# Performance work log

Measured on AMD Instinct MI355X. Metric: run time of the kernel, lower is better.

Reference implementation:

```python
import jax, jax.numpy as jnp
import numpy as np


def setup_inputs() -> dict:
    key = jax.random.key(0)
    k1, k2, k3 = jax.random.split(key, 3)
    B, C, T = 16, 256, 1024
    inp = jax.random.normal(k1, (B, C, T), dtype=jnp.float32)
    tgt = jax.random.normal(k2, (B, C, T), dtype=jnp.float32)
    mask = jax.random.uniform(k3, (B, T), dtype=jnp.float32)
    return {"inp": inp, "tgt": tgt, "mask": mask}


def reference(inp, tgt, mask):
    # inp, tgt: (B, C, T); mask: (B, T)
    # permute(0,2,1) -> (B, T, C), then mask along T
    x = jnp.transpose(inp, (0, 2, 1)) * mask[:, :, None]  # (B, T, C)
    y = jnp.transpose(tgt, (0, 2, 1)) * mask[:, :, None]  # (B, T, C)
    xy = jnp.einsum('btc,bsc->bts', x, y)  # (B, T, T)
    xx = jnp.einsum('btc,bsc->bts', x, x)  # (B, T, T)
    yy = jnp.einsum('btc,bsc->bts', y, y)  # (B, T, T)
    similarity = 2.0 * xy / (xx + yy)
    loss = jnp.exp(-similarity)
    return jnp.mean(loss)
```

## Files before the change

kernel.cpp:

```cpp
#include <hip/hip_runtime.h>

constexpr int Bc = 16;
constexpr int Cc = 256;
constexpr int Tc = 1024;

typedef __attribute__((ext_vector_type(16))) float f32x16;

__global__ void zero_out_kernel(float* out) { out[0] = 0.0f; }

__device__ inline unsigned f2fp8(float x) {
    unsigned u = __float_as_uint(x);
    unsigned sign = (u >> 24) & 0x80u;
    unsigned au = u & 0x7fffffffu;
    if (au < 0x3c800000u) {
        float m = __uint_as_float(au) * 512.0f;
        unsigned d = (unsigned)(m + 0.5f);
        return (d > 7u) ? (sign | 0x08u) : (sign | d);
    }
    if (au > 0x43e00000u) au = 0x43e00000u;
    au += 0x7ffffu + ((au >> 20) & 1u);
    unsigned e = (au >> 23) - 120u;
    return sign | (e << 3) | ((au >> 20) & 7u);
}

__global__ __launch_bounds__(256) void convert_fp8_kernel(
    const float* __restrict__ inp, const float* __restrict__ tgt,
    unsigned char* __restrict__ PX, unsigned char* __restrict__ PY,
    float* __restrict__ out)
{
    if (blockIdx.x == 0 && threadIdx.x == 0) out[0] = 0.0f;

    __shared__ float tile[32][132];
    const int gid = blockIdx.x;
    const int a  = gid >> 10;
    const int b  = (gid >> 6) & 15;
    const int cs = (gid >> 3) & 7;
    const int tg = gid & 7;
    const int t0 = tg * 128;
    const int tid = threadIdx.x;

    const float* src = a ? tgt : inp;
    unsigned char* dst = a ? PY : PX;

#pragma unroll
    for (int i = 0; i < 4; ++i) {
        const int c  = i * 8 + (tid >> 5);
        const int t4 = (tid & 31) * 4;
        const float4 v = *(const float4*)&src[((size_t)(b * Cc + cs * 32 + c)) * Tc + t0 + t4];
        tile[c][t4 + 0] = v.x; tile[c][t4 + 1] = v.y;
        tile[c][t4 + 2] = v.z; tile[c][t4 + 3] = v.w;
    }
    __syncthreads();

    const int tb  = tid >> 6;
    const int kh  = (tid >> 5) & 1;
    const int row = tid & 31;
    const int t   = tb * 32 + row;
    unsigned un[4];
#pragma unroll
    for (int q = 0; q < 4; ++q) {
        unsigned wv = 0;
#pragma unroll
        for (int jj = 0; jj < 4; ++jj) {
            const int j  = q * 4 + jj;
            const int cp = kh * 8 + (j & 7) + (j >> 3) * 16;
            wv |= f2fp8(tile[cp][t]) << (jj * 8);
        }
        un[q] = wv;
    }
    const size_t off = ((size_t)((b * 8 + cs) * 32 + tg * 4 + tb)) * 1024
                     + kh * 512 + row * 16;
    *(uint4*)(dst + off) = make_uint4(un[0], un[1], un[2], un[3]);
}

#define GLDS16(g, l) __builtin_amdgcn_global_load_lds(               \
    (__attribute__((address_space(1))) void*)(g),                    \
    (__attribute__((address_space(3))) void*)(l), 16, 0, 0)

#define MF(a, b, c) c = __builtin_amdgcn_mfma_f32_32x32x16_fp8_fp8((a), (b), (c), 0, 0, 0)

__device__ inline float epi_sum(const f32x16& XY, const f32x16& SS) {
    float l = 0.0f;
#pragma unroll
    for (int i = 0; i < 16; ++i) {
        float s = 2.0f * XY[i] / SS[i];
        s = fminf(fmaxf(s, -60.0f), 60.0f);
        l += __expf(-s);
    }
    return l;
}

__global__ __launch_bounds__(256, 2) void jvs_fp8_kernel(
    const unsigned char* __restrict__ PX,
    const unsigned char* __restrict__ PY,
    float* __restrict__ out)
{
    __shared__ __align__(16) unsigned char lds[2][16384];

    const int gid = blockIdx.x;
    const int b   = gid >> 6;
    const int tb0 = ((gid >> 3) & 7) * 4;
    const int sb0 = (gid & 7) * 4;

    const int tid  = threadIdx.x;
    const int lane = tid & 63;
    const int w    = tid >> 6;
    const int wm   = (w >> 1) * 2;
    const int wn   = (w & 1) * 2;

    const unsigned char* gax = PX + ((size_t)(b * 8 * 32 + tb0)) * 1024 + tid * 16;
    const unsigned char* gay = PY + ((size_t)(b * 8 * 32 + tb0)) * 1024 + tid * 16;
    const unsigned char* gbx = PX + ((size_t)(b * 8 * 32 + sb0)) * 1024 + tid * 16;
    const unsigned char* gby = PY + ((size_t)(b * 8 * 32 + sb0)) * 1024 + tid * 16;

    const int fo = (lane >> 5) * 512 + (lane & 31) * 16;

    f32x16 z;
#pragma unroll
    for (int i = 0; i < 16; ++i) z[i] = 0.0f;
    f32x16 xy00 = z, xy01 = z, xy10 = z, xy11 = z;
    f32x16 ss00 = z, ss01 = z, ss10 = z, ss11 = z;

#define STAGE(bufi, cs)                                               \
    do {                                                              \
        unsigned char* L = lds[bufi];                                 \
        const size_t o = (size_t)(cs) * 32768;                        \
        GLDS16(gax + o, L +     0 + tid * 16);                        \
        GLDS16(gay + o, L +  4096 + tid * 16);                        \
        GLDS16(gbx + o, L +  8192 + tid * 16);                        \
        GLDS16(gby + o, L + 12288 + tid * 16);                        \
    } while (0)

    STAGE(0, 0);
    __syncthreads();

    for (int it = 0; it < 8; ++it) {
        if (it < 7) STAGE((it + 1) & 1, it + 1);
        const unsigned char* L = lds[it & 1];

        const long2 ax0 = *(const long2*)&L[(wm + 0) * 1024 + fo];
        const long2 ax1 = *(const long2*)&L[(wm + 1) * 1024 + fo];
        const long2 ay0 = *(const long2*)&L[4096 + (wm + 0) * 1024 + fo];
        const long2 ay1 = *(const long2*)&L[4096 + (wm + 1) * 1024 + fo];
        const long2 bx0 = *(const long2*)&L[8192 + (wn + 0) * 1024 + fo];
        const long2 bx1 = *(const long2*)&L[8192 + (wn + 1) * 1024 + fo];
        const long2 by0 = *(const long2*)&L[12288 + (wn + 0) * 1024 + fo];
        const long2 by1 = *(const long2*)&L[12288 + (wn + 1) * 1024 + fo];

        MF(ax0.x, bx0.x, ss00); MF(ax0.x, bx1.x, ss01);
        MF(ax1.x, bx0.x, ss10); MF(ax1.x, bx1.x, ss11);
        MF(ay0.x, by0.x, ss00); MF(ay0.x, by1.x, ss01);
        MF(ay1.x, by0.x, ss10); MF(ay1.x, by1.x, ss11);
        MF(ax0.x, by0.x, xy00); MF(ax0.x, by1.x, xy01);
        MF(ax1.x, by0.x, xy10); MF(ax1.x, by1.x, xy11);
        MF(ax0.y, bx0.y, ss00); MF(ax0.y, bx1.y, ss01);
        MF(ax1.y, bx0.y, ss10); MF(ax1.y, bx1.y, ss11);
        MF(ay0.y, by0.y, ss00); MF(ay0.y, by1.y, ss01);
        MF(ay1.y, by0.y, ss10); MF(ay1.y, by1.y, ss11);
        MF(ax0.y, by0.y, xy00); MF(ax0.y, by1.y, xy01);
        MF(ax1.y, by0.y, xy10); MF(ax1.y, by1.y, xy11);

        __syncthreads();
    }
#undef STAGE

    float local = epi_sum(xy00, ss00) + epi_sum(xy01, ss01)
                + epi_sum(xy10, ss10) + epi_sum(xy11, ss11);

#pragma unroll
    for (int off = 32; off > 0; off >>= 1)
        local += __shfl_down(local, off, 64);

    __shared__ float red[4];
    if (lane == 0) red[w] = local;
    __syncthreads();
    if (tid == 0)
        atomicAdd(out, (red[0] + red[1] + red[2] + red[3])
                       * (1.0f / ((float)Bc * (float)Tc * (float)Tc)));
}

constexpr int TILE = 64;
constexpr int KC   = 16;

__global__ __launch_bounds__(256) void jvs_loss_kernel(
    const float* __restrict__ inp, const float* __restrict__ tgt, float* __restrict__ out)
{
    __shared__ float xs_t[KC][TILE];
    __shared__ float xs_s[KC][TILE];
    __shared__ float ys_t[KC][TILE];
    __shared__ float ys_s[KC][TILE];

    constexpr int NT = Tc / TILE;
    const int blk = blockIdx.x;
    const int b   = blk / (NT * NT);
    const int r   = blk % (NT * NT);
    const int t0  = (r / NT) * TILE;
    const int s0  = (r % NT) * TILE;
    const int tid = threadIdx.x;
    const int tx  = tid & 15;
    const int ty  = tid >> 4;
    const int lrow  = tid >> 4;
    const int lcol4 = tid & 15;
    const float* baseI = inp + (size_t)b * Cc * Tc;
    const float* baseT = tgt + (size_t)b * Cc * Tc;

    float acc_xy[4][4] = {{0.f}}, acc_xx[4][4] = {{0.f}}, acc_yy[4][4] = {{0.f}};
    for (int c0 = 0; c0 < Cc; c0 += KC) {
        __syncthreads();
        const size_t rowOff = (size_t)(c0 + lrow) * Tc;
        *(float4*)&xs_t[lrow][lcol4 * 4] = *(const float4*)(baseI + rowOff + t0 + lcol4 * 4);
        *(float4*)&xs_s[lrow][lcol4 * 4] = *(const float4*)(baseI + rowOff + s0 + lcol4 * 4);
        *(float4*)&ys_t[lrow][lcol4 * 4] = *(const float4*)(baseT + rowOff + t0 + lcol4 * 4);
        *(float4*)&ys_s[lrow][lcol4 * 4] = *(const float4*)(baseT + rowOff + s0 + lcol4 * 4);
        __syncthreads();
#pragma unroll
        for (int kc = 0; kc < KC; ++kc) {
            float xt[4], xsv[4], yt[4], ysv[4];
#pragma unroll
            for (int i = 0; i < 4; ++i) {
                xt[i]  = xs_t[kc][ty * 4 + i];  yt[i]  = ys_t[kc][ty * 4 + i];
                xsv[i] = xs_s[kc][tx * 4 + i];  ysv[i] = ys_s[kc][tx * 4 + i];
            }
#pragma unroll
            for (int i = 0; i < 4; ++i)
#pragma unroll
                for (int j = 0; j < 4; ++j) {
                    acc_xy[i][j] += xt[i] * ysv[j];
                    acc_xx[i][j] += xt[i] * xsv[j];
                    acc_yy[i][j] += yt[i] * ysv[j];
                }
        }
    }
    float local = 0.0f;
#pragma unroll
    for (int i = 0; i < 4; ++i)
#pragma unroll
        for (int j = 0; j < 4; ++j) {
            float sim = 2.0f * acc_xy[i][j] / (acc_xx[i][j] + acc_yy[i][j]);
            sim = fminf(fmaxf(sim, -60.0f), 60.0f);
            local += __expf(-sim);
        }
#pragma unroll
    for (int off = 32; off > 0; off >>= 1) local += __shfl_down(local, off, 64);
    __shared__ float red[4];
    if ((tid & 63) == 0) red[tid >> 6] = local;
    __syncthreads();
    if (tid == 0)
        atomicAdd(out, (red[0] + red[1] + red[2] + red[3])
                       * (1.0f / ((float)Bc * (float)Tc * (float)Tc)));
}

extern "C" void kernel_launch(void* const* d_in, const int* in_sizes, int n_in,
                              void* d_out, int out_size, void* d_ws, size_t ws_size,
                              hipStream_t stream) {
    const float* inp = (const float*)d_in[0];
    const float* tgt = (const float*)d_in[1];
    float* out = (float*)d_out;

    const size_t oneP = (size_t)Bc * Cc * Tc;
    if (ws_size >= 2 * oneP) {
        unsigned char* PX = (unsigned char*)d_ws;
        unsigned char* PY = PX + oneP;
        convert_fp8_kernel<<<2048, 256, 0, stream>>>(inp, tgt, PX, PY, out);
        jvs_fp8_kernel<<<1024, 256, 0, stream>>>(PX, PY, out);
    } else {
        zero_out_kernel<<<1, 1, 0, stream>>>(out);
        jvs_loss_kernel<<<Bc * (Tc / TILE) * (Tc / TILE), 256, 0, stream>>>(inp, tgt, out);
    }
}
```

Before: 105.8 us.

## Shrink fp8 MFMA tile to 64x64, load full K into LDS, XCD-aware block mapping

Restructures the fp8 similarity kernel: each block now computes a 64x64 output tile instead of 128x128. It loads the whole 256-channel K slab for its A and B tiles into 64KB of LDS in one shot, replacing the double-buffered staged loop. Blocks are remapped so each XCD handles two batches, for L2 locality. Grid size grows 4x and each wave keeps separate xx/yy/xy accumulators. This trades per-block data reuse and more global traffic for more parallelism and no pipeline syncs. The 64KB LDS per block limits occupancy.

```diff
diff --git a/kernel.cpp b/kernel.cpp
--- a/kernel.cpp
+++ b/kernel.cpp
@@ -95,83 +95,67 @@
     const unsigned char* __restrict__ PY,
     float* __restrict__ out)
 {
-    __shared__ __align__(16) unsigned char lds[2][16384];
-
-    const int gid = blockIdx.x;
-    const int b   = gid >> 6;
-    const int tb0 = ((gid >> 3) & 7) * 4;
-    const int sb0 = (gid & 7) * 4;
+    __shared__ __align__(16) unsigned char lds[65536];
+
+    const int xcd = blockIdx.x & 7;
+    const int idx = blockIdx.x >> 3;
+    const int b   = xcd * 2 + (idx >> 8);
+    const int r   = idx & 255;
+    const int tb  = r >> 4;
+    const int sb  = r & 15;
 
     const int tid  = threadIdx.x;
     const int lane = tid & 63;
     const int w    = tid >> 6;
-    const int wm   = (w >> 1) * 2;
-    const int wn   = (w & 1) * 2;
-
-    const unsigned char* gax = PX + ((size_t)(b * 8 * 32 + tb0)) * 1024 + tid * 16;
-    const unsigned char* gay = PY + ((size_t)(b * 8 * 32 + tb0)) * 1024 + tid * 16;
-    const unsigned char* gbx = PX + ((size_t)(b * 8 * 32 + sb0)) * 1024 + tid * 16;
-    const unsigned char* gby = PY + ((size_t)(b * 8 * 32 + sb0)) * 1024 + tid * 16;
+    const int wm   = w >> 1;
+    const int wn   = w & 1;
+
+    const int t4    = tid >> 6;
+    const int inner = (tid & 63) * 16;
+#pragma unroll
+    for (int i = 0; i < 4; ++i) {
+        const int tix = i * 4 + t4;
+        const int cs  = tix & 7;
+        const int m   = tix >> 3;
+        const size_t goA = ((size_t)((b * 8 + cs) * 32 + tb * 2 + m)) * 1024 + inner;
+        const size_t goB = ((size_t)((b * 8 + cs) * 32 + sb * 2 + m)) * 1024 + inner;
+        GLDS16(PX + goA, lds +     0 + i * 4096 + tid * 16);
+        GLDS16(PY + goA, lds + 16384 + i * 4096 + tid * 16);
+        GLDS16(PX + goB, lds + 32768 + i * 4096 + tid * 16);
+        GLDS16(PY + goB, lds + 49152 + i * 4096 + tid * 16);
+    }
+    __syncthreads();
 
     const int fo = (lane >> 5) * 512 + (lane & 31) * 16;
+    const int ao = (wm * 8) * 1024 + fo;
+    const int bo = (wn * 8) * 1024 + fo;
 
     f32x16 z;
 #pragma unroll
     for (int i = 0; i < 16; ++i) z[i] = 0.0f;
-    f32x16 xy00 = z, xy01 = z, xy10 = z, xy11 = z;
-    f32x16 ss00 = z, ss01 = z, ss10 = z, ss11 = z;
-
-#define STAGE(bufi, cs)                                               \
-    do {                                                              \
-        unsigned char* L = lds[bufi];                                 \
-        const size_t o = (size_t)(cs) * 32768;                        \
-        GLDS16(gax + o, L +     0 + tid * 16);                        \
-        GLDS16(gay + o, L +  4096 + tid * 16);                        \
-        GLDS16(gbx + o, L +  8192 + tid * 16);                        \
-        GLDS16(gby + o, L + 12288 + tid * 16);                        \
-    } while (0)
-
-    STAGE(0, 0);
-    __syncthreads();
-
-    for (int it = 0; it < 8; ++it) {
-        if (it < 7) STAGE((it + 1) & 1, it + 1);
-        const unsigned char* L = lds[it & 1];
-
-        const long2 ax0 = *(const long2*)&L[(wm + 0) * 1024 + fo];
-        const long2 ax1 = *(const long2*)&L[(wm + 1) * 1024 + fo];
-        const long2 ay0 = *(const long2*)&L[4096 + (wm + 0) * 1024 + fo];
-        const long2 ay1 = *(const long2*)&L[4096 + (wm + 1) * 1024 + fo];
-        const long2 bx0 = *(const long2*)&L[8192 + (wn + 0) * 1024 + fo];
-        const long2 bx1 = *(const long2*)&L[8192 + (wn + 1) * 1024 + fo];
-        const long2 by0 = *(const long2*)&L[12288 + (wn + 0) * 1024 + fo];
-        const long2 by1 = *(const long2*)&L[12288 + (wn + 1) * 1024 + fo];
-
-        MF(ax0.x, bx0.x, ss00); MF(ax0.x, bx1.x, ss01);
-        MF(ax1.x, bx0.x, ss10); MF(ax1.x, bx1.x, ss11);
-        MF(ay0.x, by0.x, ss00); MF(ay0.x, by1.x, ss01);
-        MF(ay1.x, by0.x, ss10); MF(ay1.x, by1.x, ss11);
-        MF(ax0.x, by0.x, xy00); MF(ax0.x, by1.x, xy01);
-        MF(ax1.x, by0.x, xy10); MF(ax1.x, by1.x, xy11);
-        MF(ax0.y, bx0.y, ss00); MF(ax0.y, bx1.y, ss01);
-        MF(ax1.y, bx0.y, ss10); MF(ax1.y, bx1.y, ss11);
-        MF(ay0.y, by0.y, ss00); MF(ay0.y, by1.y, ss01);
-        MF(ay1.y, by0.y, ss10); MF(ay1.y, by1.y, ss11);
-        MF(ax0.y, by0.y, xy00); MF(ax0.y, by1.y, xy01);
-        MF(ax1.y, by0.y, xy10); MF(ax1.y, by1.y, xy11);
-
-        __syncthreads();
-    }
-#undef STAGE
-
-    float local = epi_sum(xy00, ss00) + epi_sum(xy01, ss01)
-                + epi_sum(xy10, ss10) + epi_sum(xy11, ss11);
+    f32x16 xy = z, xx = z, yy = z;
+
+#pragma unroll
+    for (int cs = 0; cs < 8; ++cs) {
+        const long2 ax = *(const long2*)&lds[        ao + cs * 1024];
+        const long2 ay = *(const long2*)&lds[16384 + ao + cs * 1024];
+        const long2 bx = *(const long2*)&lds[32768 + bo + cs * 1024];
+        const long2 by = *(const long2*)&lds[49152 + bo + cs * 1024];
+        MF(ax.x, bx.x, xx); MF(ay.x, by.x, yy); MF(ax.x, by.x, xy);
+        MF(ax.y, bx.y, xx); MF(ay.y, by.y, yy); MF(ax.y, by.y, xy);
+    }
+
+    f32x16 ss;
+#pragma unroll
+    for (int i = 0; i < 16; ++i) ss[i] = xx[i] + yy[i];
+    float local = epi_sum(xy, ss);
 
 #pragma unroll
     for (int off = 32; off > 0; off >>= 1)
         local += __shfl_down(local, off, 64);
 
-    __shared__ float red[4];
+    __syncthreads();
+    float* red = (float*)lds;
     if (lane == 0) red[w] = local;
     __syncthreads();
     if (tid == 0)
@@ -262,7 +246,7 @@
         unsigned char* PX = (unsigned char*)d_ws;
         unsigned char* PY = PX + oneP;
         convert_fp8_kernel<<<2048, 256, 0, stream>>>(inp, tgt, PX, PY, out);
-        jvs_fp8_kernel<<<1024, 256, 0, stream>>>(PX, PY, out);
+        jvs_fp8_kernel<<<4096, 256, 0, stream>>>(PX, PY, out);
     } else {
         zero_out_kernel<<<1, 1, 0, stream>>>(out);
         jvs_loss_kernel<<<Bc * (Tc / TILE) * (Tc / TILE), 256, 0, stream>>>(inp, tgt, out);
```

Result: slower. 135.6 us (+28.1%).
